# Optimization experiments

Measured on AMD Instinct MI355X. Metric: run time of the kernel, lower is better.

Reference implementation:

```python
import jax, jax.numpy as jnp
from jax import lax
import numpy as np

B, C, H, W, R = 8, 256, 88, 88, 8
EPS = 1e-5

def _conv(x, w, b, stride=1, pad=0):
    out = lax.conv_general_dilated(x, w, (stride, stride), ((pad, pad), (pad, pad)),
                                   dimension_numbers=('NCHW', 'OIHW', 'NCHW'))
    return out + b[None, :, None, None]

def _bn(x, g, b, m, v):
    # eval-mode BatchNorm2d with running stats
    inv = g * lax.rsqrt(v + EPS)
    return (x - m[None, :, None, None]) * inv[None, :, None, None] + b[None, :, None, None]

def _ln_ch(x, g, b):
    # LayerNorm over the channel dim of an NCHW tensor (torch permutes to NHWC, LN, permute back)
    m = x.mean(axis=1, keepdims=True)
    var = ((x - m) ** 2).mean(axis=1, keepdims=True)
    return (x - m) * lax.rsqrt(var + EPS) * g[None, :, None, None] + b[None, :, None, None]

def _sra(qf, kvf, qw, qb, kw, kb, vw, vb, srw, srb, lng, lnb):
    # SpatialReductionAttention with reduction_ratio R > 1
    Bq, Cq, Hq, Wq = qf.shape
    Q = _conv(qf, qw, qb).reshape(Bq, Cq // 8, Hq * Wq)          # (B, C/8, N)
    kvr = _ln_ch(_conv(kvf, srw, srb, stride=R), lng, lnb)        # (B, C, H/R, W/R)
    K = _conv(kvr, kw, kb).reshape(Bq, Cq // 8, -1)               # (B, C/8, Nr)
    V = _conv(kvr, vw, vb).reshape(Bq, Cq, -1)                    # (B, C, Nr)
    scale = (Cq // 8) ** -0.5
    attn = jax.nn.softmax(jnp.einsum('bcn,bcm->bnm', Q, K) * scale, axis=-1)  # (B, N, Nr)
    return jnp.einsum('bcm,bnm->bcn', V, attn).reshape(Bq, Cq, Hq, Wq)


def setup_inputs() -> dict:
    key = jax.random.key(0)
    ks = iter(jax.random.split(key, 64))
    def nrm(shape, s=0.05):
        return jax.random.normal(next(ks), shape, dtype=jnp.float32) * s
    d = {}
    d['f_rgb'] = nrm((B, C, H, W), 1.0)
    d['f_depth'] = nrm((B, C, H, W), 1.0)
    Ct = 2 * C
    d['sm_w1'] = nrm((Ct // 2, Ct, 3, 3)); d['sm_b1'] = jnp.zeros((Ct // 2,))
    d['sm_g1'] = jnp.ones((Ct // 2,)); d['sm_be1'] = jnp.zeros((Ct // 2,))
    d['sm_m1'] = jnp.zeros((Ct // 2,)); d['sm_v1'] = jnp.ones((Ct // 2,))
    d['sm_w2'] = nrm((1, Ct // 2, 1, 1)); d['sm_b2'] = jnp.zeros((1,))
    for pfx in ('d2r', 'r2d'):
        d[pfx + '_q_w'] = nrm((C // 8, C, 1, 1)); d[pfx + '_q_b'] = jnp.zeros((C // 8,))
        d[pfx + '_k_w'] = nrm((C // 8, C, 1, 1)); d[pfx + '_k_b'] = jnp.zeros((C // 8,))
        d[pfx + '_v_w'] = nrm((C, C, 1, 1)); d[pfx + '_v_b'] = jnp.zeros((C,))
        d[pfx + '_sr_w'] = nrm((C, C, R, R), 0.02); d[pfx + '_sr_b'] = jnp.zeros((C,))
        d[pfx + '_ln_g'] = jnp.ones((C,)); d[pfx + '_ln_b'] = jnp.zeros((C,))
        d[pfx + '_norm_g'] = jnp.ones((C,)); d[pfx + '_norm_b'] = jnp.zeros((C,))
    d['d2r_gamma'] = jnp.full((1,), 0.1, dtype=jnp.float32)
    d['r2d_gamma'] = jnp.full((1,), 0.1, dtype=jnp.float32)
    Cf = 2 * C + 1
    d['fus_w'] = nrm((C, Cf, 3, 3)); d['fus_b'] = jnp.zeros((C,))
    d['fus_g'] = jnp.ones((C,)); d['fus_be'] = jnp.zeros((C,))
    d['fus_m'] = jnp.zeros((C,)); d['fus_v'] = jnp.ones((C,))
    return d


def reference(f_rgb, f_depth,
              sm_w1, sm_b1, sm_g1, sm_be1, sm_m1, sm_v1, sm_w2, sm_b2,
              d2r_q_w, d2r_q_b, d2r_k_w, d2r_k_b, d2r_v_w, d2r_v_b,
              d2r_sr_w, d2r_sr_b, d2r_ln_g, d2r_ln_b, d2r_norm_g, d2r_norm_b,
              r2d_q_w, r2d_q_b, r2d_k_w, r2d_k_b, r2d_v_w, r2d_v_b,
              r2d_sr_w, r2d_sr_b, r2d_ln_g, r2d_ln_b, r2d_norm_g, r2d_norm_b,
              d2r_gamma, r2d_gamma,
              fus_w, fus_b, fus_g, fus_be, fus_m, fus_v):
    # align_depth is Identity (depth_channels == rgb_channels), same spatial size
    concat = jnp.concatenate([f_rgb, f_depth], axis=1)
    h1 = jax.nn.relu(_bn(_conv(concat, sm_w1, sm_b1, pad=1), sm_g1, sm_be1, sm_m1, sm_v1))
    spatial_mask = jax.nn.sigmoid(_conv(h1, sm_w2, sm_b2))            # (B, 1, H, W)
    f_depth_masked = f_depth * spatial_mask

    out_d2r = _sra(f_rgb, f_depth_masked, d2r_q_w, d2r_q_b, d2r_k_w, d2r_k_b,
                   d2r_v_w, d2r_v_b, d2r_sr_w, d2r_sr_b, d2r_ln_g, d2r_ln_b)
    out_d2r = _ln_ch(out_d2r, d2r_norm_g, d2r_norm_b)
    f_rgb_enh = f_rgb + jnp.clip(d2r_gamma, 0.0, 1.0) * out_d2r

    out_r2d = _sra(f_depth_masked, f_rgb, r2d_q_w, r2d_q_b, r2d_k_w, r2d_k_b,
                   r2d_v_w, r2d_v_b, r2d_sr_w, r2d_sr_b, r2d_ln_g, r2d_ln_b)
    out_r2d = _ln_ch(out_r2d, r2d_norm_g, r2d_norm_b)
    f_depth_enh = f_depth + jnp.clip(r2d_gamma, 0.0, 1.0) * out_r2d

    fus_in = jnp.concatenate([f_rgb_enh, f_depth_enh, spatial_mask], axis=1)
    return jax.nn.relu(_bn(_conv(fus_in, fus_w, fus_b, pad=1), fus_g, fus_be, fus_m, fus_v))
```

## Files before the change

kernel.cpp:

```cpp
#include <hip/hip_runtime.h>
#include <hip/hip_bf16.h>


typedef __bf16 bf16x8 __attribute__((ext_vector_type(8)));
typedef float f32x4 __attribute__((ext_vector_type(4)));

#define AS1 __attribute__((address_space(1)))
#define AS3 __attribute__((address_space(3)))
#define DEVI __device__ __forceinline__

DEVI float bf2f(unsigned short u){
  union { unsigned int i; float f; } v; v.i = ((unsigned int)u) << 16; return v.f;
}
DEVI unsigned short f2bf(float f){
  union { float f; unsigned int i; } v; v.f = f;
  unsigned int x = v.i;
  unsigned int r = (x + 0x7fffu + ((x >> 16) & 1u)) >> 16;
  return (unsigned short)r;
}

__global__ void bnprep_k(const float* __restrict__ g1, const float* __restrict__ be1,
                         const float* __restrict__ m1, const float* __restrict__ v1,
                         const float* __restrict__ b1,
                         const float* __restrict__ gf, const float* __restrict__ bef,
                         const float* __restrict__ mf, const float* __restrict__ vf,
                         const float* __restrict__ bf,
                         float* __restrict__ sc1, float* __restrict__ sh1,
                         float* __restrict__ scf, float* __restrict__ shf)
{
  int c = threadIdx.x;
  float s = g1[c] * rsqrtf(v1[c] + 1e-5f);
  sc1[c] = s; sh1[c] = (b1[c] - m1[c]) * s + be1[c];
  s = gf[c] * rsqrtf(vf[c] + 1e-5f);
  scf[c] = s; shf[c] = (bf[c] - mf[c]) * s + bef[c];
}

__global__ __launch_bounds__(128)
void zero_border_k(unsigned short* __restrict__ buf, int px_el)
{
  int bi = blockIdx.x;
  int img = bi / 356, e = bi - img * 356;
  int y, x;
  if (e < 90){ y = 0; x = e; }
  else if (e < 180){ y = 89; x = e - 90; }
  else if (e < 268){ y = e - 180 + 1; x = 0; }
  else { y = e - 268 + 1; x = 89; }
  size_t pix = ((size_t)img * 90 + y) * 90 + x;
  int t = threadIdx.x;
  if (t < (px_el >> 3))
    *reinterpret_cast<uint4*>(buf + pix * px_el + t * 8) = uint4{0, 0, 0, 0};
}
__global__ __launch_bounds__(256)
void zero_fustail_k(unsigned short* __restrict__ FusPad)
{
  int idx = blockIdx.x * 256 + threadIdx.x;
  int n = idx >> 3, ch = idx & 7;
  int b = n / 7744, s = n - b * 7744;
  int y = s / 88, x = s - y * 88;
  size_t pix = ((size_t)(b * 90 + y + 1)) * 90 + (x + 1);
  *reinterpret_cast<uint4*>(FusPad + pix * 576 + 512 + ch * 8) = uint4{0, 0, 0, 0};
}

__global__ __launch_bounds__(256)
void prep_xpad_k(const float* __restrict__ rgb, const float* __restrict__ dep,
                 unsigned short* __restrict__ Xpad)
{
  __shared__ unsigned short tile[64][65];
  int bi = blockIdx.x;
  int b = bi / 968;
  int rem = bi - b * 968;
  int cblk = rem / 121;
  int pblk = rem - cblk * 121;
  int t = threadIdx.x;
  int pl = t & 63;
  #pragma unroll
  for (int pass = 0; pass < 16; ++pass){
    int cl = pass * 4 + (t >> 6);
    int c = cblk * 64 + cl;
    const float* sp = (c < 256) ? (rgb + ((size_t)b * 256 + c) * 7744)
                                : (dep + ((size_t)b * 256 + (c - 256)) * 7744);
    tile[cl][pl] = f2bf(sp[pblk * 64 + pl]);
  }
  __syncthreads();
  int cl2 = t & 63;
  for (int pass = 0; pass < 16; ++pass){
    int pl2 = pass * 4 + (t >> 6);
    int pixg = pblk * 64 + pl2;
    int y = pixg / 88, x = pixg - y * 88;
    Xpad[(((size_t)b * 90 + y + 1) * 90 + (x + 1)) * 512 + cblk * 64 + cl2] = tile[cl2][pl2];
  }
}

__global__ __launch_bounds__(256)
void prep_w1t_k(const float* __restrict__ w, unsigned short* __restrict__ o)
{
  int co = blockIdx.x, t = threadIdx.x;
  const float* src = w + (size_t)co * 4608 + t * 18;
  unsigned int* op = (unsigned int*)o;
  #pragma unroll
  for (int k = 0; k < 9; ++k){
    unsigned short lo = f2bf(src[k]);
    unsigned short hi = f2bf(src[9 + k]);
    op[((size_t)k * 256 + co) * 256 + t] = lo | ((unsigned int)hi << 16);
  }
}
__global__ __launch_bounds__(256)
void prep_wfus_k(const float* __restrict__ w, unsigned short* __restrict__ o)
{
  int co = blockIdx.x, t = threadIdx.x;
  const float* src = w + (size_t)co * 4617 + t * 18;
  unsigned int* op = (unsigned int*)o;
  #pragma unroll
  for (int k = 0; k < 9; ++k){
    unsigned short lo = f2bf(src[k]);
    unsigned short hi = f2bf(src[9 + k]);
    op[((size_t)k * 256 + co) * 288 + t] = lo | ((unsigned int)hi << 16);
  }
  if (t < 32){
    #pragma unroll
    for (int k = 0; k < 9; ++k){
      unsigned int val = 0;
      if (t == 0) val = (unsigned int)f2bf(w[(size_t)co * 4617 + 512 * 9 + k]);
      op[((size_t)k * 256 + co) * 288 + 256 + t] = val;
    }
  }
}
__global__ __launch_bounds__(256)
void prep_wsr_k(const float* __restrict__ w, unsigned short* __restrict__ o)
{
  __shared__ float ld[64][65];
  int co = blockIdx.x;
  int t = threadIdx.x;
  for (int cib = 0; cib < 256; cib += 64){
    int cil = t >> 2, tq = t & 3;
    const float* src = w + ((size_t)co * 256 + cib + cil) * 64 + tq * 16;
    float v[16];
    #pragma unroll
    for (int k = 0; k < 16; ++k) v[k] = src[k];
    __syncthreads();
    #pragma unroll
    for (int k = 0; k < 16; ++k) ld[cil][tq * 16 + k] = v[k];
    __syncthreads();
    #pragma unroll
    for (int tp = 0; tp < 16; ++tp){
      int tap = tp * 4 + (t >> 6);
      int ci = t & 63;
      o[((size_t)tap * 256 + co) * 256 + cib + ci] = f2bf(ld[ci][tap]);
    }
  }
}
__global__ __launch_bounds__(256)
void tranw_k(const float* __restrict__ in, unsigned short* __restrict__ out, int R, int C)
{
  __shared__ float tl[32][33];
  int tiles_c = C >> 5;
  int tr = (blockIdx.x / tiles_c) << 5, tc = (blockIdx.x % tiles_c) << 5;
  int t = threadIdx.x; int r = t >> 5, c = t & 31;
  #pragma unroll
  for (int p = 0; p < 4; ++p)
    tl[r + p * 8][c] = in[(size_t)(tr + r + p * 8) * C + tc + c];
  __syncthreads();
  #pragma unroll
  for (int p = 0; p < 4; ++p)
    out[(size_t)(tc + r + p * 8) * R + tr + c] = f2bf(tl[c][r + p * 8]);
}
__global__ __launch_bounds__(256)
void wqprep_k(const float* __restrict__ w, unsigned short* __restrict__ o)
{
  int co = blockIdx.x, t = threadIdx.x;
  int c = t >> 3, e = t & 7;
  o[co * 256 + ((c ^ (co & 7)) * 8) + e] = f2bf(w[co * 256 + t]);
}

struct GemmP {
  const unsigned short* A;
  const unsigned short* W;
  const float* ep_scale;
  const float* ep_shift;
  void* out;
  int img_px, row_px, px_el, ch_off, y0, x0;
  int tapw, stridepix, out_w, out_imgpx;
  int Cin, Mtot, Mtiles, Ntiles, k_per;
};

template<int EPI>
__global__ __launch_bounds__(256)
void gemm_k(GemmP p)
{
  __shared__ __bf16 As[128 * 64];
  __shared__ __bf16 Bs[128 * 64];
  const int t = threadIdx.x;
  const int lane = t & 63;
  const int wid = t >> 6;
  const int wr = wid >> 1, wc = wid & 1;

  const int cpx = gridDim.x >> 3;
  int pid = (blockIdx.x & 7) * cpx + (blockIdx.x >> 3);
  const int mn = p.Mtiles * p.Ntiles;
  int within = pid % mn;
  int slot = pid / mn;
  int mt = within / p.Ntiles;
  int nt = within - mt * p.Ntiles;
  int kb = slot * p.k_per;
  int tap0 = kb / p.Cin;
  int ntap = p.k_per / p.Cin;

  long long apix[4]; int cbg8[4]; int wrow[4];
  #pragma unroll
  for (int i = 0; i < 4; ++i){
    int r = i * 32 + (t >> 3);
    cbg8[i] = ((t & 7) ^ (r & 7)) * 8;
    int n = mt * 128 + r;
    int nc = n < p.Mtot ? n : 0;
    int b = nc / p.out_imgpx; int rr = nc - b * p.out_imgpx;
    int yo = rr / p.out_w;    int xo = rr - yo * p.out_w;
    apix[i] = (long long)b * p.img_px + (long long)(yo * p.stridepix + p.y0) * p.row_px
            + (xo * p.stridepix + p.x0);
    wrow[i] = (nt * 128 + r) * p.Cin + cbg8[i];
  }

  f32x4 acc[4][4];
  #pragma unroll
  for (int i = 0; i < 4; ++i)
    #pragma unroll
    for (int j = 0; j < 4; ++j)
      acc[i][j] = f32x4{0.f, 0.f, 0.f, 0.f};

  const long long wstap = 256LL * p.Cin;

  for (int cib = 0; cib < p.Cin; cib += 64){
    for (int tp = 0; tp < ntap; ++tp){
      int tap = tap0 + tp;
      int dy = tap / p.tapw, dx = tap - dy * p.tapw;
      const unsigned short* wb = p.W + (long long)tap * wstap + cib;
      const long long aoff = (long long)(dy * p.row_px + dx) * p.px_el + p.ch_off + cib;
      __syncthreads();
      #pragma unroll
      for (int i = 0; i < 4; ++i){
        __builtin_amdgcn_global_load_lds(
            (AS1 void*)(p.A + apix[i] * p.px_el + aoff + cbg8[i]),
            (AS3 void*)(&As[i * 2048 + wid * 512]),
            16, 0, 0);
        __builtin_amdgcn_global_load_lds(
            (AS1 void*)(wb + wrow[i]),
            (AS3 void*)(&Bs[i * 2048 + wid * 512]),
            16, 0, 0);
      }
      __syncthreads();
      #pragma unroll
      for (int ks = 0; ks < 2; ++ks){
        bf16x8 av[4], bv[4];
        #pragma unroll
        for (int mi = 0; mi < 4; ++mi){
          int ar = wr * 64 + mi * 16 + (lane & 15);
          int cb = (ks * 4 + (lane >> 4)) ^ (ar & 7);
          av[mi] = *reinterpret_cast<const bf16x8*>(&As[ar * 64 + cb * 8]);
        }
        #pragma unroll
        for (int ni = 0; ni < 4; ++ni){
          int br = wc * 64 + ni * 16 + (lane & 15);
          int cb = (ks * 4 + (lane >> 4)) ^ (br & 7);
          bv[ni] = *reinterpret_cast<const bf16x8*>(&Bs[br * 64 + cb * 8]);
        }
        #pragma unroll
        for (int mi = 0; mi < 4; ++mi)
          #pragma unroll
          for (int ni = 0; ni < 4; ++ni)
            acc[mi][ni] = __builtin_amdgcn_mfma_f32_16x16x32_bf16(av[mi], bv[ni], acc[mi][ni], 0, 0, 0);
      }
    }
  }

  const int r0 = (lane >> 4) * 4;
  const int c0 = lane & 15;
  #pragma unroll
  for (int mi = 0; mi < 4; ++mi){
    int nbase = mt * 128 + wr * 64 + mi * 16 + r0;
    #pragma unroll
    for (int ni = 0; ni < 4; ++ni){
      int co = nt * 128 + wc * 64 + ni * 16 + c0;
      f32x4 a = acc[mi][ni];
      if constexpr (EPI == 0){
        float sc = p.ep_scale[co], sh = p.ep_shift[co];
        unsigned short* o = (unsigned short*)p.out;
        #pragma unroll
        for (int r = 0; r < 4; ++r){
          float v = fmaf(a[r], sc, sh); v = v > 0.f ? v : 0.f;
          o[(size_t)(nbase + r) * 256 + co] = f2bf(v);
        }
      } else if constexpr (EPI == 1){
        float sc = p.ep_scale[co], sh = p.ep_shift[co];
        float* o = (float*)p.out;
        int b = nbase / 7744; int s = nbase - b * 7744;
        float4 v;
        v.x = fmaxf(fmaf(a[0], sc, sh), 0.f);
        v.y = fmaxf(fmaf(a[1], sc, sh), 0.f);
        v.z = fmaxf(fmaf(a[2], sc, sh), 0.f);
        v.w = fmaxf(fmaf(a[3], sc, sh), 0.f);
        *reinterpret_cast<float4*>(o + ((size_t)(b * 256 + co)) * 7744 + s) = v;
      } else {
        float* o = (float*)p.out + (size_t)slot * 968 * 256;
        #pragma unroll
        for (int r = 0; r < 4; ++r){
          int n = nbase + r;
          if (n < p.Mtot) o[(size_t)n * 256 + co] = a[r];
        }
      }
    }
  }
}

__global__ __launch_bounds__(256)
void mask_k(const unsigned short* __restrict__ h1, const float* __restrict__ w2,
            const float* __restrict__ b2, float* __restrict__ mask,
            unsigned short* __restrict__ FusPad)
{
  __shared__ float w[256];
  int t = threadIdx.x;
  w[t] = w2[t];
  __syncthreads();
  int n = blockIdx.x * 256 + t;
  const unsigned short* row = h1 + (size_t)n * 256;
  float s = b2[0];
  for (int c = 0; c < 256; c += 8){
    union { uint4 v; unsigned short s_[8]; } u;
    u.v = *reinterpret_cast<const uint4*>(row + c);
    #pragma unroll
    for (int j = 0; j < 8; ++j) s = fmaf(bf2f(u.s_[j]), w[c + j], s);
  }
  float m = 1.f / (1.f + __expf(-s));
  mask[n] = m;
  int b = n / 7744, sr = n - b * 7744;
  int y = sr / 88, x = sr - y * 88;
  FusPad[(((size_t)b * 90 + y + 1) * 90 + (x + 1)) * 576 + 512] = f2bf(m);
}

__global__ __launch_bounds__(256)
void fdm_k(const unsigned short* __restrict__ Xpad, const float* __restrict__ mask,
           unsigned short* __restrict__ fdm)
{
  int idx = blockIdx.x * 256 + threadIdx.x;
  int n = idx >> 5, cb = idx & 31;
  int b = n / 7744, s = n - b * 7744;
  int y = s / 88, x = s - y * 88;
  size_t pix = ((size_t)(b * 90 + y + 1)) * 90 + x + 1;
  union { uint4 v; unsigned short s_[8]; } u, w;
  u.v = *reinterpret_cast<const uint4*>(Xpad + pix * 512 + 256 + cb * 8);
  float m = mask[n];
  #pragma unroll
  for (int j = 0; j < 8; ++j) w.s_[j] = f2bf(bf2f(u.s_[j]) * m);
  *reinterpret_cast<uint4*>(fdm + (size_t)n * 256 + cb * 8) = w.v;
}

__global__ __launch_bounds__(256)
void lnkvr_k(const float* __restrict__ part, const float* __restrict__ srb,
             const float* __restrict__ lng, const float* __restrict__ lnb,
             unsigned short* __restrict__ kvr)
{
  int n = blockIdx.x, t = threadIdx.x;
  float v = srb[t];
  for (int s = 0; s < 16; ++s) v += part[((size_t)s * 968 + n) * 256 + t];
  float s1 = v, s2 = v * v;
  #pragma unroll
  for (int o = 1; o < 64; o <<= 1){ s1 += __shfl_xor(s1, o, 64); s2 += __shfl_xor(s2, o, 64); }
  __shared__ float a1[4], a2[4];
  if ((t & 63) == 0){ a1[t >> 6] = s1; a2[t >> 6] = s2; }
  __syncthreads();
  float t1 = a1[0] + a1[1] + a1[2] + a1[3];
  float t2 = a2[0] + a2[1] + a2[2] + a2[3];
  float mean = t1 * (1.f / 256.f);
  float var = t2 * (1.f / 256.f) - mean * mean;
  float rstd = rsqrtf(var + 1e-5f);
  kvr[(size_t)n * 256 + t] = f2bf((v - mean) * rstd * lng[t] + lnb[t]);
}

__global__ __launch_bounds__(256)
void dotconv_k(const unsigned short* __restrict__ src,
               const unsigned short* __restrict__ wt, const float* __restrict__ bias,
               float* __restrict__ out)
{
  __shared__ unsigned short wl[256 * 32];
  const int t = threadIdx.x;
  {
    uint4* d = (uint4*)wl; const uint4* s = (const uint4*)wt;
    #pragma unroll
    for (int k = 0; k < 4; ++k) d[t + 256 * k] = s[t + 256 * k];
  }
  __syncthreads();
  const int n = blockIdx.x * 8 + (t >> 5);
  const int co = t & 31;
  const unsigned short* row = src + (size_t)n * 256;
  float sum = bias[co];
  for (int c = 0; c < 256; c += 8){
    union { uint4 v; unsigned short s_[8]; } u;
    u.v = *reinterpret_cast<const uint4*>(row + c);
    #pragma unroll
    for (int j = 0; j < 8; ++j)
      sum = fmaf(bf2f(u.s_[j]), bf2f(wl[(c + j) * 32 + co]), sum);
  }
  out[(size_t)n * 32 + co] = sum;
}

__global__ __launch_bounds__(256)
void vconv_k(const unsigned short* __restrict__ kvr, const unsigned short* __restrict__ vwt,
             const float* __restrict__ vb, unsigned short* __restrict__ VBt)
{
  __shared__ float rowf[256];
  const int n = blockIdx.x, t = threadIdx.x;
  rowf[t] = bf2f(kvr[(size_t)n * 256 + t]);
  __syncthreads();
  float sum = vb[t];
  #pragma unroll 8
  for (int c = 0; c < 256; ++c)
    sum = fmaf(rowf[c], bf2f(vwt[(size_t)c * 256 + t]), sum);
  int b = n / 121, m = n - b * 121;
  VBt[(size_t)b * 32768 + (size_t)t * 128 + m] = f2bf(sum);
}

__global__ __launch_bounds__(512, 2)
void attn_k(const unsigned short* __restrict__ Qsrc, int qmode,
            const unsigned short* __restrict__ wq, const float* __restrict__ qb,
            const float* __restrict__ Kbuf,
            const unsigned short* __restrict__ VBt,
            const unsigned short* __restrict__ Xpad, int resChOff,
            unsigned short* __restrict__ FusPad, int outChOff,
            const float* __restrict__ ng, const float* __restrict__ nbv,
            const float* __restrict__ gammap)
{
  __shared__ unsigned short Vt[2][256][64];
  __shared__ unsigned short Pl[2][128][64];
  __shared__ unsigned short Qs[128][64];
  __shared__ unsigned short Ks[128][64];
  __shared__ unsigned short Wqs[32][256];

  const int t = threadIdx.x;
  const int lane = t & 63;
  const int w = t >> 6;
  const int c15 = lane & 15;
  const int h = lane >> 4;

  const int bid = blockIdx.x;
  const int b = bid / 61;
  const int rb = bid - b * 61;
  const int nb0 = rb * 128;

  const unsigned short* vsrc = VBt + (size_t)b * 32768;
  #pragma unroll
  for (int kt = 0; kt < 2; ++kt)
    #pragma unroll
    for (int i = 0; i < 4; ++i){
      int rowbase = i * 64 + w * 8;
      int c = rowbase + (lane >> 3);
      int mchunk = (lane & 7) ^ (c & 7);
      __builtin_amdgcn_global_load_lds(
        (AS1 void*)(vsrc + (size_t)c * 128 + kt * 64 + mchunk * 8),
        (AS3 void*)(&Vt[kt][rowbase][0]),
        16, 0, 0);
    }

  {
    uint4* d = (uint4*)&Wqs[0][0]; const uint4* s = (const uint4*)wq;
    d[t] = s[t];
    d[t + 512] = s[t + 512];
  }
  {
    int m = t >> 2, part = t & 3;
    union { uint4 v; unsigned short s_[8]; } u;
    u.v = uint4{0, 0, 0, 0};
    if (m < 121){
      const float* kp = Kbuf + ((size_t)b * 121 + m) * 32 + part * 8;
      float4 a = *reinterpret_cast<const float4*>(kp);
      float4 bb = *reinterpret_cast<const float4*>(kp + 4);
      u.s_[0] = f2bf(a.x); u.s_[1] = f2bf(a.y); u.s_[2] = f2bf(a.z); u.s_[3] = f2bf(a.w);
      u.s_[4] = f2bf(bb.x); u.s_[5] = f2bf(bb.y); u.s_[6] = f2bf(bb.z); u.s_[7] = f2bf(bb.w);
    }
    *reinterpret_cast<uint4*>(&Ks[m][(part ^ (m & 7)) * 8]) = u.v;
  }
  __syncthreads();

  const int nA = w * 16 + c15;
  const float scale = 0.17677669529663687f;

  {
    int gn = nb0 + nA; if (gn > 7743) gn = 7743;
    const unsigned short* xrow;
    if (qmode){
      int y = gn / 88, x = gn - y * 88;
      xrow = Qsrc + (((size_t)(b * 90) + y + 1) * 90 + (x + 1)) * 512;
    } else {
      xrow = Qsrc + ((size_t)b * 7744 + gn) * 256;
    }
    f32x4 qacc[2];
    qacc[0] = f32x4{0.f, 0.f, 0.f, 0.f};
    qacc[1] = f32x4{0.f, 0.f, 0.f, 0.f};
    #pragma unroll
    for (int kt = 0; kt < 8; ++kt){
      bf16x8 ax = *reinterpret_cast<const bf16x8*>(xrow + kt * 32 + h * 8);
      #pragma unroll
      for (int ni = 0; ni < 2; ++ni){
        int co = ni * 16 + c15;
        bf16x8 bw = *reinterpret_cast<const bf16x8*>(&Wqs[co][((kt * 4 + h) ^ (co & 7)) * 8]);
        qacc[ni] = __builtin_amdgcn_mfma_f32_16x16x32_bf16(ax, bw, qacc[ni], 0, 0, 0);
      }
    }
    #pragma unroll
    for (int ni = 0; ni < 2; ++ni){
      int co = ni * 16 + c15;
      float bq = qb[co];
      #pragma unroll
      for (int r = 0; r < 4; ++r){
        int n = w * 16 + 4 * h + r;
        int chunk = (co >> 3) ^ (n & 7);
        Qs[n][chunk * 8 + (co & 7)] = f2bf((qacc[ni][r] + bq) * scale);
      }
    }
  }

  bf16x8 aq = *reinterpret_cast<const bf16x8*>(&Qs[nA][(h ^ (nA & 7)) * 8]);
  f32x4 sv[8];
  #pragma unroll
  for (int ni = 0; ni < 8; ++ni){
    int mrow = ni * 16 + c15;
    bf16x8 bk = *reinterpret_cast<const bf16x8*>(&Ks[mrow][(h ^ (mrow & 7)) * 8]);
    sv[ni] = __builtin_amdgcn_mfma_f32_16x16x32_bf16(aq, bk, f32x4{0.f,0.f,0.f,0.f}, 0, 0, 0);
  }
  if (c15 >= 9) sv[7] = f32x4{-1e30f, -1e30f, -1e30f, -1e30f};

  float rden[4];
  #pragma unroll
  for (int r = 0; r < 4; ++r){
    float mx = sv[0][r];
    #pragma unroll
    for (int ni = 1; ni < 8; ++ni) mx = fmaxf(mx, sv[ni][r]);
    #pragma unroll
    for (int o = 1; o < 16; o <<= 1) mx = fmaxf(mx, __shfl_xor(mx, o, 64));
    float sm = 0.f;
    #pragma unroll
    for (int ni = 0; ni < 8; ++ni){
      float p = __expf(sv[ni][r] - mx);
      sv[ni][r] = p;
      sm += p;
    }
    #pragma unroll
    for (int o = 1; o < 16; o <<= 1) sm += __shfl_xor(sm, o, 64);
    rden[r] = 1.f / sm;
  }
  #pragma unroll
  for (int ni = 0; ni < 8; ++ni){
    int m = ni * 16 + c15;
    int kt = m >> 6;
    int mq = (m & 63) >> 3;
    #pragma unroll
    for (int r = 0; r < 4; ++r){
      int n = w * 16 + 4 * h + r;
      Pl[kt][n][(mq ^ (n & 7)) * 8 + (m & 7)] = f2bf(sv[ni][r] * rden[r]);
    }
  }

  bf16x8 pa[2][2];
  #pragma unroll
  for (int kt = 0; kt < 2; ++kt)
    #pragma unroll
    for (int ks = 0; ks < 2; ++ks)
      pa[kt][ks] = *reinterpret_cast<const bf16x8*>(&Pl[kt][nA][((ks * 4 + h) ^ (nA & 7)) * 8]);

  f32x4 acc[16];
  #pragma unroll
  for (int ni = 0; ni < 16; ++ni) acc[ni] = f32x4{0.f, 0.f, 0.f, 0.f};
  #pragma unroll
  for (int ni = 0; ni < 16; ++ni){
    int crow = ni * 16 + c15;
    #pragma unroll
    for (int kt = 0; kt < 2; ++kt)
      #pragma unroll
      for (int ks = 0; ks < 2; ++ks){
        bf16x8 bv = *reinterpret_cast<const bf16x8*>(&Vt[kt][crow][((ks * 4 + h) ^ (crow & 7)) * 8]);
        acc[ni] = __builtin_amdgcn_mfma_f32_16x16x32_bf16(pa[kt][ks], bv, acc[ni], 0, 0, 0);
      }
  }

  float ngv[16], nbb[16];
  #pragma unroll
  for (int ni = 0; ni < 16; ++ni){
    int c = ni * 16 + c15;
    ngv[ni] = ng[c]; nbb[ni] = nbv[c];
  }
  float g = gammap[0]; g = fminf(fmaxf(g, 0.f), 1.f);

  #pragma unroll
  for (int r = 0; r < 4; ++r){
    float s1 = 0.f, s2 = 0.f;
    #pragma unroll
    for (int ni = 0; ni < 16; ++ni){ float v = acc[ni][r]; s1 += v; s2 += v * v; }
    #pragma unroll
    for (int o = 1; o < 16; o <<= 1){ s1 += __shfl_xor(s1, o, 64); s2 += __shfl_xor(s2, o, 64); }
    float mean = s1 * (1.f / 256.f);
    float var = s2 * (1.f / 256.f) - mean * mean;
    float rstd = rsqrtf(var + 1e-5f);

    int nloc = w * 16 + 4 * h + r;
    int rix = nb0 + nloc;
    if (rix < 7744){
      int y = rix / 88, x = rix - y * 88;
      size_t pix = ((size_t)(b * 90) + y + 1) * 90 + (x + 1);
      const unsigned short* res = Xpad + pix * 512 + resChOff;
      unsigned short* outp = FusPad + pix * 576 + outChOff;
      #pragma unroll
      for (int ni = 0; ni < 16; ++ni){
        int c = ni * 16 + c15;
        float yv = (acc[ni][r] - mean) * rstd * ngv[ni] + nbb[ni];
        outp[c] = f2bf(bf2f(res[c]) + g * yv);
      }
    }
  }
}

extern "C" void kernel_launch(void* const* d_in, const int* in_sizes, int n_in,
                              void* d_out, int out_size, void* d_ws, size_t ws_size,
                              hipStream_t stream)
{
  const float* P[42];
  for (int i = 0; i < 42; ++i) P[i] = (const float*)d_in[i];

  char* ws = (char*)d_ws;
  size_t off = 0;
  auto take = [&](size_t bytes) -> char* {
    char* p = ws + off; off += (bytes + 255) & ~(size_t)255; return p;
  };
  unsigned short* XPAD = (unsigned short*)take(8ull * 8100 * 512 * 2);
  unsigned short* FUSP = (unsigned short*)take(8ull * 8100 * 576 * 2);
  unsigned short* H1   = (unsigned short*)take(61952ull * 256 * 2);
  unsigned short* FDM  = H1;
  unsigned short* W1T  = (unsigned short*)take(9ull * 256 * 512 * 2);
  unsigned short* WFT  = (unsigned short*)take(9ull * 256 * 576 * 2);
  unsigned short* WSRA = (unsigned short*)take(64ull * 256 * 256 * 2);
  unsigned short* WSRB = (unsigned short*)take(64ull * 256 * 256 * 2);
  float* PART = (float*)take(16ull * 968 * 256 * 4);
  unsigned short* KVR = (unsigned short*)take(968ull * 256 * 2);
  float* KB   = (float*)take(968ull * 32 * 4);
  unsigned short* VBT = (unsigned short*)take(8ull * 256 * 128 * 2);
  float* MASK = (float*)take(61952ull * 4);
  float* SC1 = (float*)take(256 * 4);
  float* SH1 = (float*)take(256 * 4);
  float* SCF = (float*)take(256 * 4);
  float* SHF = (float*)take(256 * 4);
  unsigned short* WQSA = (unsigned short*)take(32ull * 256 * 2);
  unsigned short* WQSB = (unsigned short*)take(32ull * 256 * 2);
  unsigned short* KWTA = (unsigned short*)take(256ull * 32 * 2);
  unsigned short* VWTA = (unsigned short*)take(256ull * 256 * 2);
  unsigned short* KWTB = (unsigned short*)take(256ull * 32 * 2);
  unsigned short* VWTB = (unsigned short*)take(256ull * 256 * 2);
  (void)ws_size; (void)in_sizes; (void)n_in; (void)out_size;

  zero_border_k<<<8 * 356, 128, 0, stream>>>(XPAD, 512);
  zero_border_k<<<8 * 356, 128, 0, stream>>>(FUSP, 576);
  zero_fustail_k<<<1936, 256, 0, stream>>>(FUSP);
  hipMemsetAsync(VBT, 0, 8ull * 256 * 128 * 2, stream);

  bnprep_k<<<1, 256, 0, stream>>>(P[4], P[5], P[6], P[7], P[3],
                                  P[38], P[39], P[40], P[41], P[37],
                                  SC1, SH1, SCF, SHF);
  prep_xpad_k<<<7744, 256, 0, stream>>>(P[0], P[1], XPAD);
  prep_w1t_k<<<256, 256, 0, stream>>>(P[2], W1T);
  prep_wfus_k<<<256, 256, 0, stream>>>(P[36], WFT);
  prep_wsr_k<<<256, 256, 0, stream>>>(P[16], WSRA);
  prep_wsr_k<<<256, 256, 0, stream>>>(P[28], WSRB);
  wqprep_k<<<32, 256, 0, stream>>>(P[10], WQSA);
  wqprep_k<<<32, 256, 0, stream>>>(P[22], WQSB);
  tranw_k<<<8, 256, 0, stream>>>(P[12], KWTA, 32, 256);
  tranw_k<<<64, 256, 0, stream>>>(P[14], VWTA, 256, 256);
  tranw_k<<<8, 256, 0, stream>>>(P[24], KWTB, 32, 256);
  tranw_k<<<64, 256, 0, stream>>>(P[26], VWTB, 256, 256);

  GemmP g1{};
  g1.A = XPAD; g1.W = W1T; g1.ep_scale = SC1; g1.ep_shift = SH1; g1.out = H1;
  g1.img_px = 8100; g1.row_px = 90; g1.px_el = 512; g1.ch_off = 0; g1.y0 = 0; g1.x0 = 0;
  g1.tapw = 3; g1.stridepix = 1; g1.out_w = 88; g1.out_imgpx = 7744;
  g1.Cin = 512; g1.Mtot = 61952; g1.Mtiles = 484; g1.Ntiles = 2; g1.k_per = 4608;
  gemm_k<0><<<968, 256, 0, stream>>>(g1);

  mask_k<<<242, 256, 0, stream>>>(H1, P[8], P[9], MASK, FUSP);
  fdm_k<<<7744, 256, 0, stream>>>(XPAD, MASK, FDM);

  GemmP gs{};
  gs.A = FDM; gs.W = WSRA; gs.out = PART;
  gs.img_px = 7744; gs.row_px = 88; gs.px_el = 256; gs.ch_off = 0; gs.y0 = 0; gs.x0 = 0;
  gs.tapw = 8; gs.stridepix = 8; gs.out_w = 11; gs.out_imgpx = 121;
  gs.Cin = 256; gs.Mtot = 968; gs.Mtiles = 8; gs.Ntiles = 2; gs.k_per = 1024;
  gemm_k<2><<<256, 256, 0, stream>>>(gs);
  lnkvr_k<<<968, 256, 0, stream>>>(PART, P[17], P[18], P[19], KVR);
  dotconv_k<<<121, 256, 0, stream>>>(KVR, KWTA, P[13], KB);
  vconv_k<<<968, 256, 0, stream>>>(KVR, VWTA, P[15], VBT);
  attn_k<<<488, 512, 0, stream>>>(XPAD, 1, WQSA, P[11], KB, VBT, XPAD, 0,
                                  FUSP, 0, P[20], P[21], P[34]);

  gs.A = XPAD; gs.W = WSRB;
  gs.img_px = 8100; gs.row_px = 90; gs.px_el = 512; gs.y0 = 1; gs.x0 = 1;
  gemm_k<2><<<256, 256, 0, stream>>>(gs);
  lnkvr_k<<<968, 256, 0, stream>>>(PART, P[29], P[30], P[31], KVR);
  dotconv_k<<<121, 256, 0, stream>>>(KVR, KWTB, P[25], KB);
  vconv_k<<<968, 256, 0, stream>>>(KVR, VWTB, P[27], VBT);
  attn_k<<<488, 512, 0, stream>>>(FDM, 0, WQSB, P[23], KB, VBT, XPAD, 256,
                                  FUSP, 256, P[32], P[33], P[35]);

  GemmP gf{};
  gf.A = FUSP; gf.W = WFT; gf.ep_scale = SCF; gf.ep_shift = SHF; gf.out = d_out;
  gf.img_px = 8100; gf.row_px = 90; gf.px_el = 576; gf.ch_off = 0; gf.y0 = 0; gf.x0 = 0;
  gf.tapw = 3; gf.stridepix = 1; gf.out_w = 88; gf.out_imgpx = 7744;
  gf.Cin = 576; gf.Mtot = 61952; gf.Mtiles = 484; gf.Ntiles = 2; gf.k_per = 5184;
  gemm_k<1><<<968, 256, 0, stream>>>(gf);
}
```

Measured before the change: 615.0 us.

## Double-buffer LDS tiles in conv GEMM to overlap global loads with MFMA

Turns the A/B shared-memory tiles into two buffers so the next k-step's global_load_lds is issued before the current tile's MFMAs run. Hand-placed s_waitcnt vmcnt and s_barrier calls replace the two __syncthreads per k-step. The intent is to hide global memory latency behind compute. This doubles LDS use to 64 KB per block, which may lower occupancy.

```diff
diff --git a/kernel.cpp b/kernel.cpp
--- a/kernel.cpp
+++ b/kernel.cpp
@@ -187,8 +187,8 @@
 __global__ __launch_bounds__(256)
 void gemm_k(GemmP p)
 {
-  __shared__ __bf16 As[128 * 64];
-  __shared__ __bf16 Bs[128 * 64];
+  __shared__ __bf16 As[2][128 * 64];
+  __shared__ __bf16 Bs[2][128 * 64];
   const int t = threadIdx.x;
   const int lane = t & 63;
   const int wid = t >> 6;
@@ -228,47 +228,65 @@
 
   const long long wstap = 256LL * p.Cin;
 
-  for (int cib = 0; cib < p.Cin; cib += 64){
-    for (int tp = 0; tp < ntap; ++tp){
-      int tap = tap0 + tp;
-      int dy = tap / p.tapw, dx = tap - dy * p.tapw;
-      const unsigned short* wb = p.W + (long long)tap * wstap + cib;
-      const long long aoff = (long long)(dy * p.row_px + dx) * p.px_el + p.ch_off + cib;
-      __syncthreads();
+  auto STAGE = [&](int buf, int tap, int cib){
+    int dy = tap / p.tapw, dx = tap - dy * p.tapw;
+    const unsigned short* wb = p.W + (long long)tap * wstap + cib;
+    const long long aoff = (long long)(dy * p.row_px + dx) * p.px_el + p.ch_off + cib;
+    #pragma unroll
+    for (int i = 0; i < 4; ++i){
+      __builtin_amdgcn_global_load_lds(
+          (AS1 void*)(p.A + apix[i] * p.px_el + aoff + cbg8[i]),
+          (AS3 void*)(&As[buf][i * 2048 + wid * 512]),
+          16, 0, 0);
+      __builtin_amdgcn_global_load_lds(
+          (AS1 void*)(wb + wrow[i]),
+          (AS3 void*)(&Bs[buf][i * 2048 + wid * 512]),
+          16, 0, 0);
+    }
+  };
+
+  const int NT = (p.Cin >> 6) * ntap;
+  STAGE(0, tap0, 0);
+  int tpn = 1, tap_n = tap0 + 1, cib_n = 0;
+  int cur = 0;
+
+  for (int kt = 0; kt < NT; ++kt){
+    if (kt + 1 < NT){
+      STAGE(cur ^ 1, tap_n, cib_n);
+      ++tpn; ++tap_n;
+      if (tpn == ntap){ tpn = 0; tap_n = tap0; cib_n += 64; }
+      asm volatile("s_waitcnt vmcnt(8)" ::: "memory");
+    } else {
+      asm volatile("s_waitcnt vmcnt(0)" ::: "memory");
+    }
+    __builtin_amdgcn_s_barrier();
+    __builtin_amdgcn_sched_barrier(0);
+
+    #pragma unroll
+    for (int ks = 0; ks < 2; ++ks){
+      bf16x8 av[4], bv[4];
       #pragma unroll
-      for (int i = 0; i < 4; ++i){
-        __builtin_amdgcn_global_load_lds(
-            (AS1 void*)(p.A + apix[i] * p.px_el + aoff + cbg8[i]),
-            (AS3 void*)(&As[i * 2048 + wid * 512]),
-            16, 0, 0);
-        __builtin_amdgcn_global_load_lds(
-            (AS1 void*)(wb + wrow[i]),
-            (AS3 void*)(&Bs[i * 2048 + wid * 512]),
-            16, 0, 0);
+      for (int mi = 0; mi < 4; ++mi){
+        int ar = wr * 64 + mi * 16 + (lane & 15);
+        int cb = (ks * 4 + (lane >> 4)) ^ (ar & 7);
+        av[mi] = *reinterpret_cast<const bf16x8*>(&As[cur][ar * 64 + cb * 8]);
       }
-      __syncthreads();
       #pragma unroll
-      for (int ks = 0; ks < 2; ++ks){
-        bf16x8 av[4], bv[4];
+      for (int ni = 0; ni < 4; ++ni){
+        int br = wc * 64 + ni * 16 + (lane & 15);
+        int cb = (ks * 4 + (lane >> 4)) ^ (br & 7);
+        bv[ni] = *reinterpret_cast<const bf16x8*>(&Bs[cur][br * 64 + cb * 8]);
+      }
+      #pragma unroll
+      for (int mi = 0; mi < 4; ++mi)
         #pragma unroll
-        for (int mi = 0; mi < 4; ++mi){
-          int ar = wr * 64 + mi * 16 + (lane & 15);
-          int cb = (ks * 4 + (lane >> 4)) ^ (ar & 7);
-          av[mi] = *reinterpret_cast<const bf16x8*>(&As[ar * 64 + cb * 8]);
-        }
-        #pragma unroll
-        for (int ni = 0; ni < 4; ++ni){
-          int br = wc * 64 + ni * 16 + (lane & 15);
-          int cb = (ks * 4 + (lane >> 4)) ^ (br & 7);
-          bv[ni] = *reinterpret_cast<const bf16x8*>(&Bs[br * 64 + cb * 8]);
-        }
-        #pragma unroll
-        for (int mi = 0; mi < 4; ++mi)
-          #pragma unroll
-          for (int ni = 0; ni < 4; ++ni)
-            acc[mi][ni] = __builtin_amdgcn_mfma_f32_16x16x32_bf16(av[mi], bv[ni], acc[mi][ni], 0, 0, 0);
-      }
-    }
+        for (int ni = 0; ni < 4; ++ni)
+          acc[mi][ni] = __builtin_amdgcn_mfma_f32_16x16x32_bf16(av[mi], bv[ni], acc[mi][ni], 0, 0, 0);
+    }
+
+    __builtin_amdgcn_sched_barrier(0);
+    __builtin_amdgcn_s_barrier();
+    cur ^= 1;
   }
 
   const int r0 = (lane >> 4) * 4;
```

Result: faster. 599.2 us (-2.6%).
